# Kernel optimization log

Hardware: AMD Instinct MI355X
Metric: run time of the kernel (lower is better)

The kernel has to match this reference:

```python
import jax, jax.numpy as jnp
import numpy as np
import math

V, D, L, H, T, B = 32000, 1024, 4, 16, 2048, 1
HD = D // H
EPS = 1e-5

def _pos_encoding(T, D):
    pos = jnp.arange(T, dtype=jnp.float32)[:, None]                      # [T,1]
    div = jnp.exp(jnp.arange(0, D, 2, dtype=jnp.float32) * (-math.log(10000.0) / D))
    ang = pos * div                                                      # [T,D/2]
    pe = jnp.zeros((T, D), dtype=jnp.float32)
    pe = pe.at[:, 0::2].set(jnp.sin(ang)).at[:, 1::2].set(jnp.cos(ang))
    return pe

def _layernorm(x, g, b):
    mu = jnp.mean(x, axis=-1, keepdims=True)
    var = jnp.mean(jnp.square(x - mu), axis=-1, keepdims=True)
    return (x - mu) * jax.lax.rsqrt(var + EPS) * g + b

def setup_inputs() -> dict:
    key = jax.random.key(0)
    ks = jax.random.split(key, 16)
    s = 0.02
    inp = {
        'idx': jax.random.randint(ks[0], (B, T), 0, V),
        'embed': jax.random.normal(ks[1], (V, D), jnp.float32) * s,
        'Wq': jax.random.normal(ks[2], (L, D, D), jnp.float32) * s,
        'Wk': jax.random.normal(ks[3], (L, D, D), jnp.float32) * s,
        'Wv': jax.random.normal(ks[4], (L, D, D), jnp.float32) * s,
        'Wo': jax.random.normal(ks[5], (L, D, D), jnp.float32) * s,
        'bq': jnp.zeros((L, D), jnp.float32),
        'bk': jnp.zeros((L, D), jnp.float32),
        'bv': jnp.zeros((L, D), jnp.float32),
        'bo': jnp.zeros((L, D), jnp.float32),
        'ln1_g': jnp.ones((L, D), jnp.float32), 'ln1_b': jnp.zeros((L, D), jnp.float32),
        'ln2_g': jnp.ones((L, D), jnp.float32), 'ln2_b': jnp.zeros((L, D), jnp.float32),
        'w1': jax.random.normal(ks[6], (L, D, 4 * D), jnp.float32) * s,
        'b1': jnp.zeros((L, 4 * D), jnp.float32),
        'w2': jax.random.normal(ks[7], (L, 4 * D, D), jnp.float32) * s,
        'b2': jnp.zeros((L, D), jnp.float32),
        'lnf_g': jnp.ones((D,), jnp.float32), 'lnf_b': jnp.zeros((D,), jnp.float32),
        'head_w': jax.random.normal(ks[8], (D, V), jnp.float32) * s,
    }
    return inp

def _forward(idx, embed, Wq, Wk, Wv, Wo, bq, bk, bv, bo,
             ln1_g, ln1_b, ln2_g, ln2_b, w1, b1, w2, b2, lnf_g, lnf_b, head_w):
    Bs, Ts = idx.shape
    x = embed[idx] + _pos_encoding(Ts, embed.shape[1])[None]            # [B,T,D]
    causal = jnp.tril(jnp.ones((Ts, Ts), dtype=bool))                   # [T,T]
    scale = 1.0 / math.sqrt(HD)

    def block(x, p):
        wq, wk, wv, wo, q_b, k_b, v_b, o_b, g1, be1, g2, be2, fw1, fb1, fw2, fb2 = p
        h = _layernorm(x, g1, be1)
        q = (h @ wq + q_b).reshape(Bs, Ts, H, HD)
        k = (h @ wk + k_b).reshape(Bs, Ts, H, HD)
        v = (h @ wv + v_b).reshape(Bs, Ts, H, HD)
        att = jnp.einsum('bthd,bshd->bhts', q, k) * scale               # [B,H,T,T]
        att = jnp.where(causal, att, -jnp.inf)
        att = jax.nn.softmax(att, axis=-1)
        o = jnp.einsum('bhts,bshd->bthd', att, v).reshape(Bs, Ts, -1)
        x = x + (o @ wo + o_b)
        h2 = _layernorm(x, g2, be2)
        ff = jax.nn.gelu(h2 @ fw1 + fb1, approximate=False) @ fw2 + fb2
        x = x + ff
        return x, None

    params = (Wq, Wk, Wv, Wo, bq, bk, bv, bo, ln1_g, ln1_b, ln2_g, ln2_b, w1, b1, w2, b2)
    x, _ = jax.lax.scan(block, x, params)
    x = _layernorm(x, lnf_g, lnf_b)
    return x @ head_w                                                   # [B,T,V]

def reference(idx, embed, Wq, Wk, Wv, Wo, bq, bk, bv, bo,
              ln1_g, ln1_b, ln2_g, ln2_b, w1, b1, w2, b2, lnf_g, lnf_b, head_w):
    return _forward(idx, embed, Wq, Wk, Wv, Wo, bq, bk, bv, bo,
                    ln1_g, ln1_b, ln2_g, ln2_b, w1, b1, w2, b2, lnf_g, lnf_b, head_w)
```

## Files before the change

kernel.cpp:

```cpp
#include <hip/hip_runtime.h>
#include <cstdint>

using u16 = unsigned short;
using u32 = unsigned int;
typedef __bf16  bf16x8 __attribute__((ext_vector_type(8)));
typedef float   f32x4  __attribute__((ext_vector_type(4)));
typedef float   f32x16 __attribute__((ext_vector_type(16)));

__device__ __forceinline__ u16 f2b(float x) {
    u32 u = __builtin_bit_cast(u32, x);
    u = (u + 0x7fffu + ((u >> 16) & 1u)) >> 16;
    return (u16)u;
}

__device__ __forceinline__ f32x4 mfma16(bf16x8 a, bf16x8 b, f32x4 c) {
    return __builtin_amdgcn_mfma_f32_16x16x32_bf16(a, b, c, 0, 0, 0);
}
__device__ __forceinline__ f32x16 mfma32(bf16x8 a, bf16x8 b, f32x16 c) {
    return __builtin_amdgcn_mfma_f32_32x32x16_bf16(a, b, c, 0, 0, 0);
}

__device__ __forceinline__ void gload16(const void* g, void* lds) {
    auto gp = (__attribute__((address_space(1))) void*)(uintptr_t)g;
    auto lp = (__attribute__((address_space(3))) void*)(uintptr_t)lds;
    __builtin_amdgcn_global_load_lds(gp, lp, 16, 0, 0);
}

__device__ __forceinline__ int2 swz_bmbn(int nbm) {
    const int nwg = gridDim.x, orig = blockIdx.x;
    const int q = nwg >> 3, r = nwg & 7;
    const int xcd = orig & 7, lin = orig >> 3;
    const int id = (xcd < r ? xcd * (q + 1) : r * (q + 1) + (xcd - r) * q) + lin;
    return make_int2(id % nbm, id / nbm);
}

__global__ __launch_bounds__(512, 2) void gemm_head_k(
    const u16* __restrict__ A, const u16* __restrict__ Bt,
    float* __restrict__ out, int M, int N)
{
    constexpr int KV = 1024;
    constexpr int H  = KV >> 5;
    __shared__ __align__(16) u16 lsA[4][256 * 32];
    __shared__ __align__(16) u16 lsB[4][256 * 32];
    const int nbm = M >> 8;
    const int2 bb = swz_bmbn(nbm);
    const int m0 = bb.x * 256, n0 = bb.y * 256;
    const int tid = threadIdx.x;
    const int w = tid >> 6, lane = tid & 63;
    const int wr = (w >> 2) * 128, wc = (w & 3) * 64;
    const int lr = lane & 15, lg = lane >> 4;
    const int rsw = (lg ^ ((lr >> 1) & 3)) * 8;

    const int trow = tid >> 2;
    const int ksw8 = ((tid & 3) ^ ((tid >> 3) & 3)) * 8;
    const u16* aA = A  + (size_t)(m0 + trow) * KV + ksw8;
    const u16* aB = Bt + (size_t)(n0 + trow) * KV + ksw8;
    u16* dA = &lsA[0][0] + trow * 32 + (tid & 3) * 8;
    u16* dB = &lsB[0][0] + trow * 32 + (tid & 3) * 8;

    f32x4 acc[8][4] = {};

    auto stage = [&](int h) {
        const int sl = h & 3;
        const int ko = h * 32;
        gload16(aA + ko,                      dA + sl * 8192);
        gload16(aA + ko + (size_t)128 * KV,   dA + sl * 8192 + 4096);
        gload16(aB + ko,                      dB + sl * 8192);
        gload16(aB + ko + (size_t)128 * KV,   dB + sl * 8192 + 4096);
    };

    bf16x8 ra0[8], rb0[4], ra1[8], rb1[4];
    auto rdLow = [&](bf16x8* ra, bf16x8* rb, int h) {
        const int sl = h & 3;
#pragma unroll
        for (int m = 0; m < 4; m++)
            ra[m] = *(const bf16x8*)&lsA[sl][(wr + m * 16 + lr) * 32 + rsw];
#pragma unroll
        for (int n = 0; n < 4; n++)
            rb[n] = *(const bf16x8*)&lsB[sl][(wc + n * 16 + lr) * 32 + rsw];
    };
    auto rdHigh = [&](bf16x8* ra, int h) {
        const int sl = h & 3;
#pragma unroll
        for (int m = 4; m < 8; m++)
            ra[m] = *(const bf16x8*)&lsA[sl][(wr + m * 16 + lr) * 32 + rsw];
    };

    auto body = [&](int h, bf16x8* raC, bf16x8* rbC, bf16x8* raN, bf16x8* rbN) {
        rdHigh(raC, h);
        if (h + 3 < H) stage(h + 3);
        const int rem = H - 1 - h;
        if (rem >= 3)      asm volatile("s_waitcnt vmcnt(8)" ::: "memory");
        else if (rem == 2) asm volatile("s_waitcnt vmcnt(4)" ::: "memory");
        else if (rem == 1) asm volatile("s_waitcnt vmcnt(0)" ::: "memory");
        __builtin_amdgcn_s_barrier();
        asm volatile("s_waitcnt lgkmcnt(4)" ::: "memory");
        __builtin_amdgcn_sched_barrier(0);
        __builtin_amdgcn_s_setprio(1);
#pragma unroll
        for (int m = 0; m < 4; m++)
#pragma unroll
            for (int n = 0; n < 4; n++)
                acc[m][n] = mfma16(raC[m], rbC[n], acc[m][n]);
        __builtin_amdgcn_s_setprio(0);
        __builtin_amdgcn_sched_barrier(0);
        __builtin_amdgcn_s_barrier();
        if (h + 1 < H) rdLow(raN, rbN, h + 1);
        __builtin_amdgcn_sched_barrier(0);
        __builtin_amdgcn_s_barrier();
        if (h + 1 < H) asm volatile("s_waitcnt lgkmcnt(8)" ::: "memory");
        else           asm volatile("s_waitcnt lgkmcnt(0)" ::: "memory");
        __builtin_amdgcn_sched_barrier(0);
        __builtin_amdgcn_s_setprio(1);
#pragma unroll
        for (int m = 4; m < 8; m++)
#pragma unroll
            for (int n = 0; n < 4; n++)
                acc[m][n] = mfma16(raC[m], rbC[n], acc[m][n]);
        __builtin_amdgcn_s_setprio(0);
        __builtin_amdgcn_sched_barrier(0);
        __builtin_amdgcn_s_barrier();
    };

    stage(0); stage(1); stage(2);
    asm volatile("s_waitcnt vmcnt(8)" ::: "memory");
    __builtin_amdgcn_s_barrier();
    rdLow(ra0, rb0, 0);

#pragma unroll
    for (int h = 0; h < H; h += 2) {
        body(h,     ra0, rb0, ra1, rb1);
        body(h + 1, ra1, rb1, ra0, rb0);
    }

#pragma unroll
    for (int m = 0; m < 8; m++) {
        const int gr = m0 + wr + m * 16 + lg * 4;
#pragma unroll
        for (int r = 0; r < 4; r++) {
            float* orow = out + (size_t)(gr + r) * N + n0 + wc + lr;
#pragma unroll
            for (int n = 0; n < 4; n++)
                orow[n * 16] = acc[m][n][r];
        }
    }
}

template <int KC, int EPI>
__global__ __launch_bounds__(256, 2) void gemm_deep_k(
    const u16* __restrict__ A, int lda, const u16* __restrict__ Bt, int ldb,
    const float* __restrict__ bias, float* __restrict__ outf,
    u16* __restrict__ outb, int N, int nbm, int sk, long long sOut)
{
    constexpr int MF   = 4;
    constexpr int NF   = 4;
    constexpr int SLOT = 128 * 32;
    constexpr int HALF = 64 * 32;
    constexpr int H    = KC >> 5;

    __shared__ __align__(16) u16 lsA[4][SLOT];
    __shared__ __align__(16) u16 lsB[4][SLOT];

    const int s = blockIdx.y;
    A  += (size_t)s * sk;
    Bt += (size_t)s * sk;
    if (EPI == 4) outf += (size_t)s * sOut;

    const int2 bb = swz_bmbn(nbm);
    const int m0 = bb.x * 128, n0 = bb.y * 128;
    const int tid = threadIdx.x;
    const int w = tid >> 6, lane = tid & 63;
    const int wr = (w >> 1) * 64, wc = (w & 1) * 64;
    const int lr = lane & 15, lg = lane >> 4;
    const int rsw = (lg ^ ((lr >> 1) & 3)) * 8;

    const int trow = tid >> 2;
    const int ksw8 = ((tid & 3) ^ ((tid >> 3) & 3)) * 8;
    const u16* aA = A  + (size_t)(m0 + trow) * lda + ksw8;
    const u16* aB = Bt + (size_t)(n0 + trow) * ldb + ksw8;
    u16* dA = &lsA[0][0] + trow * 32 + (tid & 3) * 8;
    u16* dB = &lsB[0][0] + trow * 32 + (tid & 3) * 8;

    f32x4 acc[MF][NF] = {};

    auto stage = [&](int h) {
        const int sl = h & 3;
        const int koff = h * 32;
        gload16(aA + koff,                     dA + sl * SLOT);
        gload16(aA + koff + (size_t)64 * lda,  dA + sl * SLOT + HALF);
        gload16(aB + koff,                     dB + sl * SLOT);
        gload16(aB + koff + (size_t)64 * ldb,  dB + sl * SLOT + HALF);
    };

    bf16x8 ra0[MF], rb0[NF], ra1[MF], rb1[NF];
    auto lreadAll = [&](bf16x8* af, bf16x8* bf, int h) {
        const int sl = h & 3;
#pragma unroll
        for (int m = 0; m < MF; m++)
            af[m] = *(const bf16x8*)&lsA[sl][(wr + m * 16 + lr) * 32 + rsw];
#pragma unroll
        for (int n = 0; n < NF; n++)
            bf[n] = *(const bf16x8*)&lsB[sl][(wc + n * 16 + lr) * 32 + rsw];
    };

    auto body = [&](int h, bf16x8* aC, bf16x8* bC, bf16x8* aN, bf16x8* bN) {
        if (h + 3 < H) stage(h + 3);
        __builtin_amdgcn_sched_barrier(0);
        asm volatile("s_waitcnt lgkmcnt(0)" ::: "memory");
        const int rem = H - 1 - h;
        if (rem >= 3)      asm volatile("s_waitcnt vmcnt(8)" ::: "memory");
        else if (rem == 2) asm volatile("s_waitcnt vmcnt(4)" ::: "memory");
        else if (rem == 1) asm volatile("s_waitcnt vmcnt(0)" ::: "memory");
        __builtin_amdgcn_s_barrier();
        __builtin_amdgcn_sched_barrier(0);
        const int sl1 = (h + 1) & 3;
        const bool doRead = (h + 1 < H);
#pragma unroll
        for (int g = 0; g < 4; ++g) {
            if (doRead) {
#pragma unroll
                for (int t = g * 2; t < g * 2 + 2; ++t) {
                    if (t < MF) aN[t]      = *(const bf16x8*)&lsA[sl1][(wr + t * 16 + lr) * 32 + rsw];
                    else        bN[t - MF] = *(const bf16x8*)&lsB[sl1][(wc + (t - MF) * 16 + lr) * 32 + rsw];
                }
            }
            __builtin_amdgcn_sched_barrier(0);
            __builtin_amdgcn_s_setprio(1);
#pragma unroll
            for (int i = g * 4; i < g * 4 + 4; ++i)
                acc[i / NF][i % NF] = mfma16(aC[i / NF], bC[i % NF], acc[i / NF][i % NF]);
            __builtin_amdgcn_s_setprio(0);
            __builtin_amdgcn_sched_barrier(0);
        }
    };

    stage(0); stage(1); stage(2);
    asm volatile("s_waitcnt vmcnt(8)" ::: "memory");
    __builtin_amdgcn_s_barrier();
    lreadAll(ra0, rb0, 0);

#pragma unroll
    for (int h = 0; h < H; h += 2) {
        body(h,     ra0, rb0, ra1, rb1);
        body(h + 1, ra1, rb1, ra0, rb0);
    }

#pragma unroll
    for (int n = 0; n < NF; n++) {
        const int gc = n0 + wc + n * 16 + lr;
        float bv = 0.f;
        if constexpr (EPI == 0 || EPI == 1) bv = bias[gc];
#pragma unroll
        for (int m = 0; m < MF; m++) {
            const int grb = m0 + wr + m * 16 + lg * 4;
#pragma unroll
            for (int r = 0; r < 4; r++) {
                float v = acc[m][n][r] + bv;
                if constexpr (EPI == 1) v = 0.5f * v * (1.f + erff(v * 0.70710678118654752f));
                const size_t o = (size_t)(grb + r) * N + gc;
                if constexpr (EPI == 4) outf[o] = v;
                else                    outb[o] = f2b(v);
            }
        }
    }
}

__global__ __launch_bounds__(256) void reduce_ln_k(
    const float* __restrict__ pbuf, int S,
    const float* __restrict__ bias,
    float* __restrict__ x,
    const float* __restrict__ g, const float* __restrict__ bln,
    u16* __restrict__ hb)
{
    __shared__ float red[8];
    const int row = blockIdx.x, tid = threadIdx.x;
    const int w = tid >> 6, lane = tid & 63;
    const size_t base = (size_t)row * 256 + tid;
    float4 v = ((const float4*)x)[base];
    for (int s = 0; s < S; ++s) {
        const float4 p = ((const float4*)pbuf)[(size_t)s * 524288 + base];
        v.x += p.x; v.y += p.y; v.z += p.z; v.w += p.w;
    }
    const float4 bb = ((const float4*)bias)[tid];
    v.x += bb.x; v.y += bb.y; v.z += bb.z; v.w += bb.w;
    ((float4*)x)[base] = v;

    float s1 = v.x + v.y + v.z + v.w;
#pragma unroll
    for (int d = 1; d < 64; d <<= 1) s1 += __shfl_xor(s1, d);
    if (lane == 0) red[w] = s1;
    __syncthreads();
    const float mu = (red[0] + red[1] + red[2] + red[3]) * (1.f / 1024.f);
    const float d0 = v.x - mu, d1 = v.y - mu, d2 = v.z - mu, d3 = v.w - mu;
    float s2 = d0 * d0 + d1 * d1 + d2 * d2 + d3 * d3;
#pragma unroll
    for (int d = 1; d < 64; d <<= 1) s2 += __shfl_xor(s2, d);
    if (lane == 0) red[4 + w] = s2;
    __syncthreads();
    const float var = (red[4] + red[5] + red[6] + red[7]) * (1.f / 1024.f);
    const float rs = rsqrtf(var + 1e-5f);
    const float4 gv = ((const float4*)g)[tid];
    const float4 bv = ((const float4*)bln)[tid];
    u32 p0 = (u32)f2b(d0 * rs * gv.x + bv.x) | ((u32)f2b(d1 * rs * gv.y + bv.y) << 16);
    u32 p1 = (u32)f2b(d2 * rs * gv.z + bv.z) | ((u32)f2b(d3 * rs * gv.w + bv.w) << 16);
    ((uint2*)(hb + (size_t)row * 1024))[tid] = make_uint2(p0, p1);
}

__global__ __launch_bounds__(256) void flash_attn_k(
    const u16* __restrict__ qkv, const u16* __restrict__ vT, u16* __restrict__ out)
{
    constexpr int DS = 3072, T = 2048;
    __shared__ float mrg[2][64][32];
    __shared__ float msh[2][32], lsh[2][32];
    __shared__ u16   sbuf[2][32 * 68];
    const int w = threadIdx.x >> 6, lane = threadIdx.x & 63;
    const int lq = lane & 31, hi = lane >> 5;
    const int hoff = blockIdx.y * 64;
    const int pair = w >> 1, par = w & 1;
    const int qt = (pair == 0) ? blockIdx.x : 63 - blockIdx.x;
    const int q0 = qt * 32;
    const int qg = q0 + lq;

    const u16* qp = qkv + (size_t)qg * DS + hoff;
    const u16* kp = qkv + 1024 + hoff;

    bf16x8 qf[4];
#pragma unroll
    for (int d = 0; d < 4; d++)
        qf[d] = *(const bf16x8*)(qp + d * 16 + hi * 8);

    f32x16 o0 = {}, o1 = {};
    float m_r = -1e30f, l_r = 0.f;

    const int ntiles = (qt >> 1) + 1;
    for (int t = par; t < ntiles; t += 2) {
        const int kv0 = t * 64;
        f32x16 s0 = {}, s1 = {};
        {
            const u16* kb0 = kp + (size_t)(kv0 + lq) * DS + hi * 8;
            const u16* kb1 = kb0 + (size_t)32 * DS;
#pragma unroll
            for (int d = 0; d < 4; d++) {
                s0 = mfma32(*(const bf16x8*)(kb0 + d * 16), qf[d], s0);
                s1 = mfma32(*(const bf16x8*)(kb1 + d * 16), qf[d], s1);
            }
        }
        float p[32];
        float mx = -1e30f;
#pragma unroll
        for (int r = 0; r < 16; r++) {
            const int kvl = (r & 3) + 8 * (r >> 2) + 4 * hi;
            float v0 = (kv0 + kvl      <= qg) ? s0[r] * 0.125f : -1e30f;
            float v1 = (kv0 + 32 + kvl <= qg) ? s1[r] * 0.125f : -1e30f;
            p[r] = v0; p[16 + r] = v1;
            mx = fmaxf(mx, fmaxf(v0, v1));
        }
        mx = fmaxf(mx, __shfl_xor(mx, 32));
        const float mn = fmaxf(m_r, mx);
        const float alpha = __expf(m_r - mn);
        m_r = mn;
        float ls = 0.f;
#pragma unroll
        for (int i = 0; i < 32; i++) { p[i] = __expf(p[i] - mn); ls += p[i]; }
        ls += __shfl_xor(ls, 32);
        l_r = l_r * alpha + ls;
#pragma unroll
        for (int r = 0; r < 16; r++) { o0[r] *= alpha; o1[r] *= alpha; }
#pragma unroll
        for (int sub = 0; sub < 2; sub++) {
            u32 pw[8], x[8];
#pragma unroll
            for (int i = 0; i < 8; i++)
                pw[i] = (u32)f2b(p[sub * 16 + 2 * i]) | ((u32)f2b(p[sub * 16 + 2 * i + 1]) << 16);
#pragma unroll
            for (int i = 0; i < 8; i++) x[i] = __shfl_xor(pw[i], 32);
            u32 b0[4], b1[4];
            b0[0] = hi ? x[2]  : pw[0];  b0[1] = hi ? x[3]  : pw[1];
            b0[2] = hi ? pw[2] : x[0];   b0[3] = hi ? pw[3] : x[1];
            b1[0] = hi ? x[6]  : pw[4];  b1[1] = hi ? x[7]  : pw[5];
            b1[2] = hi ? pw[6] : x[4];   b1[3] = hi ? pw[7] : x[5];
            bf16x8 B0 = __builtin_bit_cast(bf16x8, *(const uint4*)b0);
            bf16x8 B1 = __builtin_bit_cast(bf16x8, *(const uint4*)b1);
            const u16* vb = vT + (size_t)(hoff + lq) * T + kv0 + sub * 32 + hi * 8;
            o0 = mfma32(*(const bf16x8*)vb, B0, o0);
            o0 = mfma32(*(const bf16x8*)(vb + 16), B1, o0);
            const u16* vb1 = vb + (size_t)32 * T;
            o1 = mfma32(*(const bf16x8*)vb1, B0, o1);
            o1 = mfma32(*(const bf16x8*)(vb1 + 16), B1, o1);
        }
    }

    __syncthreads();
    if (par == 0) {
#pragma unroll
        for (int r = 0; r < 16; r++) {
            const int d = (r & 3) + 8 * (r >> 2) + 4 * hi;
            mrg[pair][d][lq]      = o0[r];
            mrg[pair][d + 32][lq] = o1[r];
        }
        if (hi == 0) { msh[pair][lq] = m_r; lsh[pair][lq] = l_r; }
    }
    __syncthreads();
    if (par == 1) {
        const float m0v = msh[pair][lq], l0v = lsh[pair][lq];
        const float M = fmaxf(m0v, m_r);
        const float f0 = __expf(m0v - M), f1 = __expf(m_r - M);
        const float linv = 1.f / (l0v * f0 + l_r * f1);
        u32* sb = (u32*)sbuf[pair];
#pragma unroll
        for (int r = 0; r < 16; r += 2) {
            const int d = (r & 3) + 8 * (r >> 2) + 4 * hi;
            float va = (mrg[pair][d][lq] * f0 + o0[r] * f1) * linv;
            float vb = (mrg[pair][d + 1][lq] * f0 + o0[r + 1] * f1) * linv;
            sb[lq * 34 + (d >> 1)] = (u32)f2b(va) | ((u32)f2b(vb) << 16);
            float vc = (mrg[pair][d + 32][lq] * f0 + o1[r] * f1) * linv;
            float vd = (mrg[pair][d + 33][lq] * f0 + o1[r + 1] * f1) * linv;
            sb[lq * 34 + ((d + 32) >> 1)] = (u32)f2b(vc) | ((u32)f2b(vd) << 16);
        }
#pragma unroll
        for (int ps = 0; ps < 8; ps++) {
            const int row = ps * 4 + (lane >> 4);
            const uint2 v = *(const uint2*)&sbuf[pair][row * 68 + (lane & 15) * 4];
            *(uint2*)(out + (size_t)(q0 + row) * 1024 + hoff + (lane & 15) * 4) = v;
        }
    }
}

__global__ __launch_bounds__(256) void transpose_cvt_k(
    const float* __restrict__ src, u16* __restrict__ dst, int K, int N,
    long long srcLS, long long dstLS)
{
    __shared__ float tf[32][132];
    src += (size_t)blockIdx.z * srcLS;
    dst += (size_t)blockIdx.z * dstLS;
    const int n0 = blockIdx.x * 128, k0 = blockIdx.y * 32;
    const int tid = threadIdx.x;
    const int tn = tid & 31, tk = tid >> 5;
#pragma unroll
    for (int p = 0; p < 4; ++p) {
        const int k = tk + p * 8;
        const float4 v = *(const float4*)&src[(size_t)(k0 + k) * N + n0 + tn * 4];
        *(float4*)&tf[k][tn * 4] = v;
    }
    __syncthreads();
    const int kq = (tid & 7) * 4;
    const int tn2 = tid >> 3;
#pragma unroll
    for (int w = 0; w < 4; ++w) {
        const int n = tn2 + w * 32;
        const u32 lo = (u32)f2b(tf[kq + 0][n]) | ((u32)f2b(tf[kq + 1][n]) << 16);
        const u32 hi = (u32)f2b(tf[kq + 2][n]) | ((u32)f2b(tf[kq + 3][n]) << 16);
        *(uint2*)&dst[(size_t)(n0 + n) * K + k0 + kq] = make_uint2(lo, hi);
    }
}

__global__ __launch_bounds__(256) void transpose_u16_k(
    const u16* __restrict__ src, u16* __restrict__ dst, int R, int C, int srcStride)
{
    __shared__ u16 tile[32][33];
    const int c0 = blockIdx.x * 32, r0 = blockIdx.y * 32;
    const int tx = threadIdx.x & 31, ty = threadIdx.x >> 5;
#pragma unroll
    for (int r = 0; r < 32; r += 8)
        tile[ty + r][tx] = src[(size_t)(r0 + ty + r) * srcStride + c0 + tx];
    __syncthreads();
#pragma unroll
    for (int r = 0; r < 32; r += 8)
        dst[(size_t)(c0 + ty + r) * R + r0 + tx] = tile[tx][ty + r];
}

__global__ __launch_bounds__(256) void concat_bias_k(
    const float* __restrict__ bq, const float* __restrict__ bk,
    const float* __restrict__ bv, float* __restrict__ bcat)
{
    const int l = blockIdx.y;
    const int j = blockIdx.x * 256 + threadIdx.x;
    float v;
    if (j < 1024)      v = bq[l * 1024 + j];
    else if (j < 2048) v = bk[l * 1024 + j - 1024];
    else               v = bv[l * 1024 + j - 2048];
    bcat[l * 3072 + j] = v;
}

__global__ __launch_bounds__(256) void embed_pos_k(
    const int* __restrict__ idx, const float* __restrict__ emb, float* __restrict__ x)
{
    const int t = blockIdx.x, tid = threadIdx.x;
    const int tok = idx[t];
    float4 e = ((const float4*)(emb + (size_t)tok * 1024))[tid];
    const int d0 = tid * 4;
    const float c = -0.0089944730195080f;
    const float a0 = (float)t * expf((float)d0 * c);
    const float a1 = (float)t * expf((float)(d0 + 2) * c);
    e.x += sinf(a0); e.y += cosf(a0); e.z += sinf(a1); e.w += cosf(a1);
    ((float4*)(x + (size_t)t * 1024))[tid] = e;
}

__global__ __launch_bounds__(256) void layernorm_k(
    const float* __restrict__ x, const float* __restrict__ g,
    const float* __restrict__ b, u16* __restrict__ out)
{
    __shared__ float red[8];
    const int row = blockIdx.x, tid = threadIdx.x;
    const int w = tid >> 6, lane = tid & 63;
    const float4 v = ((const float4*)(x + (size_t)row * 1024))[tid];
    float s = v.x + v.y + v.z + v.w;
#pragma unroll
    for (int d = 1; d < 64; d <<= 1) s += __shfl_xor(s, d);
    if (lane == 0) red[w] = s;
    __syncthreads();
    const float mu = (red[0] + red[1] + red[2] + red[3]) * (1.f / 1024.f);
    const float d0 = v.x - mu, d1 = v.y - mu, d2 = v.z - mu, d3 = v.w - mu;
    float s2 = d0 * d0 + d1 * d1 + d2 * d2 + d3 * d3;
#pragma unroll
    for (int d = 1; d < 64; d <<= 1) s2 += __shfl_xor(s2, d);
    if (lane == 0) red[4 + w] = s2;
    __syncthreads();
    const float var = (red[4] + red[5] + red[6] + red[7]) * (1.f / 1024.f);
    const float rs = rsqrtf(var + 1e-5f);
    const float4 gv = ((const float4*)g)[tid];
    const float4 bv = ((const float4*)b)[tid];
    u32 p0 = (u32)f2b(d0 * rs * gv.x + bv.x) | ((u32)f2b(d1 * rs * gv.y + bv.y) << 16);
    u32 p1 = (u32)f2b(d2 * rs * gv.z + bv.z) | ((u32)f2b(d3 * rs * gv.w + bv.w) << 16);
    ((uint2*)(out + (size_t)row * 1024))[tid] = make_uint2(p0, p1);
}

extern "C" void kernel_launch(void* const* d_in, const int* in_sizes, int n_in,
                              void* d_out, int out_size, void* d_ws, size_t ws_size,
                              hipStream_t stream)
{
    const int*   idx   = (const int*)  d_in[0];
    const float* embed = (const float*)d_in[1];
    const float* Wq    = (const float*)d_in[2];
    const float* Wk    = (const float*)d_in[3];
    const float* Wv    = (const float*)d_in[4];
    const float* Wo    = (const float*)d_in[5];
    const float* bq    = (const float*)d_in[6];
    const float* bk    = (const float*)d_in[7];
    const float* bv    = (const float*)d_in[8];
    const float* bo    = (const float*)d_in[9];
    const float* ln1g  = (const float*)d_in[10];
    const float* ln1b  = (const float*)d_in[11];
    const float* ln2g  = (const float*)d_in[12];
    const float* ln2b  = (const float*)d_in[13];
    const float* w1    = (const float*)d_in[14];
    const float* b1    = (const float*)d_in[15];
    const float* w2    = (const float*)d_in[16];
    const float* b2    = (const float*)d_in[17];
    const float* lnfg  = (const float*)d_in[18];
    const float* lnfb  = (const float*)d_in[19];
    const float* headw = (const float*)d_in[20];

    char* ws = (char*)d_ws;
    auto alloc = [&](size_t bytes) {
        char* p = ws;
        ws += (bytes + 255) & ~(size_t)255;
        return p;
    };
    u16*   qkvT = (u16*)alloc((size_t)4 * 3072 * 1024 * 2);
    u16*   WoT  = (u16*)alloc((size_t)4 * 1024 * 1024 * 2);
    u16*   w1T  = (u16*)alloc((size_t)4 * 1024 * 4096 * 2);
    u16*   w2T  = (u16*)alloc((size_t)4 * 1024 * 4096 * 2);
    u16*   hT   = (u16*)alloc((size_t)32000 * 1024 * 2);
    float* bcat = (float*)alloc((size_t)4 * 3072 * 4);
    float* x    = (float*)alloc((size_t)2048 * 1024 * 4);
    u16*   hb   = (u16*)alloc((size_t)2048 * 1024 * 2);
    u16*   qkvb = (u16*)alloc((size_t)2048 * 3072 * 2);
    u16*   vTb  = (u16*)alloc((size_t)2048 * 1024 * 2);
    u16*   ab   = (u16*)alloc((size_t)2048 * 1024 * 2);
    u16*   ff   = (u16*)alloc((size_t)2048 * 4096 * 2);
    float* pbuf = (float*)d_out;

    transpose_cvt_k<<<dim3(8, 32, 4),   256, 0, stream>>>(Wq, qkvT,            1024, 1024, 1048576, 3145728);
    transpose_cvt_k<<<dim3(8, 32, 4),   256, 0, stream>>>(Wk, qkvT + 1048576,  1024, 1024, 1048576, 3145728);
    transpose_cvt_k<<<dim3(8, 32, 4),   256, 0, stream>>>(Wv, qkvT + 2097152,  1024, 1024, 1048576, 3145728);
    transpose_cvt_k<<<dim3(8, 32, 4),   256, 0, stream>>>(Wo, WoT,             1024, 1024, 1048576, 1048576);
    transpose_cvt_k<<<dim3(32, 32, 4),  256, 0, stream>>>(w1, w1T,             1024, 4096, 4194304, 4194304);
    transpose_cvt_k<<<dim3(8, 128, 4),  256, 0, stream>>>(w2, w2T,             4096, 1024, 4194304, 4194304);
    transpose_cvt_k<<<dim3(250, 32, 1), 256, 0, stream>>>(headw, hT,           1024, 32000, 0, 0);
    concat_bias_k<<<dim3(12, 4), 256, 0, stream>>>(bq, bk, bv, bcat);

    embed_pos_k<<<dim3(2048), 256, 0, stream>>>(idx, embed, x);
    layernorm_k<<<dim3(2048), 256, 0, stream>>>(x, ln1g, ln1b, hb);

    for (int l = 0; l < 4; ++l) {
        gemm_deep_k<1024, 0><<<dim3(384), 256, 0, stream>>>(
            hb, 1024, qkvT + (size_t)l * 3145728, 1024,
            bcat + l * 3072, nullptr, qkvb, 3072, 16, 0, 0);
        transpose_u16_k<<<dim3(32, 64), 256, 0, stream>>>(qkvb + 2048, vTb, 2048, 1024, 3072);
        flash_attn_k<<<dim3(32, 16), 256, 0, stream>>>(qkvb, vTb, ab);
        gemm_deep_k<512, 4><<<dim3(128, 2), 256, 0, stream>>>(
            ab, 1024, WoT + (size_t)l * 1048576, 1024,
            nullptr, pbuf, nullptr, 1024, 16, 512, 2097152);
        reduce_ln_k<<<dim3(2048), 256, 0, stream>>>(pbuf, 2, bo + l * 1024, x,
                                                    ln2g + l * 1024, ln2b + l * 1024, hb);
        gemm_deep_k<1024, 1><<<dim3(512), 256, 0, stream>>>(
            hb, 1024, w1T + (size_t)l * 4194304, 1024,
            b1 + l * 4096, nullptr, ff, 4096, 16, 0, 0);
        gemm_deep_k<1024, 4><<<dim3(128, 4), 256, 0, stream>>>(
            ff, 4096, w2T + (size_t)l * 4194304, 4096,
            nullptr, pbuf, nullptr, 1024, 16, 1024, 2097152);
        const float* ng = (l < 3) ? (ln1g + (l + 1) * 1024) : lnfg;
        const float* nb = (l < 3) ? (ln1b + (l + 1) * 1024) : lnfb;
        reduce_ln_k<<<dim3(2048), 256, 0, stream>>>(pbuf, 4, b2 + l * 1024, x, ng, nb, hb);
    }
    gemm_head_k<<<dim3(1000), 512, 0, stream>>>(hb, hT, (float*)d_out, 2048, 32000);
}
```

Measured before the change: 975.8 us.

## Simplify GEMM main-loop scheduling and fuse embedding with first layernorm

Both GEMM kernels drop their hand-interleaved LDS-read/MFMA schedule, with its split halves, extra barriers and sched_barrier groups. Each iteration now reads the whole next fragment set and then issues all MFMAs in one block, leaving the interleaving to the compiler. Separately, the embedding+positional-encoding kernel is fused with the first layernorm, which saves one launch and a reread of x. The simpler GEMM schedule removes barrier overhead but may lose the explicit overlap of LDS reads with matrix ops.

```diff
diff --git a/kernel.cpp b/kernel.cpp
--- a/kernel.cpp
+++ b/kernel.cpp
@@ -70,62 +70,42 @@
     };
 
     bf16x8 ra0[8], rb0[4], ra1[8], rb1[4];
-    auto rdLow = [&](bf16x8* ra, bf16x8* rb, int h) {
+    auto lread = [&](bf16x8* af, bf16x8* bf, int h) {
         const int sl = h & 3;
 #pragma unroll
-        for (int m = 0; m < 4; m++)
-            ra[m] = *(const bf16x8*)&lsA[sl][(wr + m * 16 + lr) * 32 + rsw];
+        for (int m = 0; m < 8; m++)
+            af[m] = *(const bf16x8*)&lsA[sl][(wr + m * 16 + lr) * 32 + rsw];
 #pragma unroll
         for (int n = 0; n < 4; n++)
-            rb[n] = *(const bf16x8*)&lsB[sl][(wc + n * 16 + lr) * 32 + rsw];
-    };
-    auto rdHigh = [&](bf16x8* ra, int h) {
-        const int sl = h & 3;
-#pragma unroll
-        for (int m = 4; m < 8; m++)
-            ra[m] = *(const bf16x8*)&lsA[sl][(wr + m * 16 + lr) * 32 + rsw];
-    };
-
-    auto body = [&](int h, bf16x8* raC, bf16x8* rbC, bf16x8* raN, bf16x8* rbN) {
-        rdHigh(raC, h);
+            bf[n] = *(const bf16x8*)&lsB[sl][(wc + n * 16 + lr) * 32 + rsw];
+    };
+    auto mm = [&](bf16x8* af, bf16x8* bf) {
+        __builtin_amdgcn_s_setprio(1);
+#pragma unroll
+        for (int m = 0; m < 8; m++)
+#pragma unroll
+            for (int n = 0; n < 4; n++)
+                acc[m][n] = mfma16(af[m], bf[n], acc[m][n]);
+        __builtin_amdgcn_s_setprio(0);
+    };
+
+    auto body = [&](int h, bf16x8* aC, bf16x8* bC, bf16x8* aN, bf16x8* bN) {
         if (h + 3 < H) stage(h + 3);
+        asm volatile("s_waitcnt lgkmcnt(0)" ::: "memory");
         const int rem = H - 1 - h;
         if (rem >= 3)      asm volatile("s_waitcnt vmcnt(8)" ::: "memory");
         else if (rem == 2) asm volatile("s_waitcnt vmcnt(4)" ::: "memory");
         else if (rem == 1) asm volatile("s_waitcnt vmcnt(0)" ::: "memory");
         __builtin_amdgcn_s_barrier();
-        asm volatile("s_waitcnt lgkmcnt(4)" ::: "memory");
         __builtin_amdgcn_sched_barrier(0);
-        __builtin_amdgcn_s_setprio(1);
-#pragma unroll
-        for (int m = 0; m < 4; m++)
-#pragma unroll
-            for (int n = 0; n < 4; n++)
-                acc[m][n] = mfma16(raC[m], rbC[n], acc[m][n]);
-        __builtin_amdgcn_s_setprio(0);
-        __builtin_amdgcn_sched_barrier(0);
-        __builtin_amdgcn_s_barrier();
-        if (h + 1 < H) rdLow(raN, rbN, h + 1);
-        __builtin_amdgcn_sched_barrier(0);
-        __builtin_amdgcn_s_barrier();
-        if (h + 1 < H) asm volatile("s_waitcnt lgkmcnt(8)" ::: "memory");
-        else           asm volatile("s_waitcnt lgkmcnt(0)" ::: "memory");
-        __builtin_amdgcn_sched_barrier(0);
-        __builtin_amdgcn_s_setprio(1);
-#pragma unroll
-        for (int m = 4; m < 8; m++)
-#pragma unroll
-            for (int n = 0; n < 4; n++)
-                acc[m][n] = mfma16(raC[m], rbC[n], acc[m][n]);
-        __builtin_amdgcn_s_setprio(0);
-        __builtin_amdgcn_sched_barrier(0);
-        __builtin_amdgcn_s_barrier();
+        if (h + 1 < H) lread(aN, bN, h + 1);
+        mm(aC, bC);
     };
 
     stage(0); stage(1); stage(2);
     asm volatile("s_waitcnt vmcnt(8)" ::: "memory");
     __builtin_amdgcn_s_barrier();
-    rdLow(ra0, rb0, 0);
+    lread(ra0, rb0, 0);
 
 #pragma unroll
     for (int h = 0; h < H; h += 2) {
@@ -193,7 +173,7 @@
     };
 
     bf16x8 ra0[MF], rb0[NF], ra1[MF], rb1[NF];
-    auto lreadAll = [&](bf16x8* af, bf16x8* bf, int h) {
+    auto lread = [&](bf16x8* af, bf16x8* bf, int h) {
         const int sl = h & 3;
 #pragma unroll
         for (int m = 0; m < MF; m++)
@@ -205,7 +185,6 @@
 
     auto body = [&](int h, bf16x8* aC, bf16x8* bC, bf16x8* aN, bf16x8* bN) {
         if (h + 3 < H) stage(h + 3);
-        __builtin_amdgcn_sched_barrier(0);
         asm volatile("s_waitcnt lgkmcnt(0)" ::: "memory");
         const int rem = H - 1 - h;
         if (rem >= 3)      asm volatile("s_waitcnt vmcnt(8)" ::: "memory");
@@ -213,31 +192,20 @@
         else if (rem == 1) asm volatile("s_waitcnt vmcnt(0)" ::: "memory");
         __builtin_amdgcn_s_barrier();
         __builtin_amdgcn_sched_barrier(0);
-        const int sl1 = (h + 1) & 3;
-        const bool doRead = (h + 1 < H);
-#pragma unroll
-        for (int g = 0; g < 4; ++g) {
-            if (doRead) {
-#pragma unroll
-                for (int t = g * 2; t < g * 2 + 2; ++t) {
-                    if (t < MF) aN[t]      = *(const bf16x8*)&lsA[sl1][(wr + t * 16 + lr) * 32 + rsw];
-                    else        bN[t - MF] = *(const bf16x8*)&lsB[sl1][(wc + (t - MF) * 16 + lr) * 32 + rsw];
-                }
-            }
-            __builtin_amdgcn_sched_barrier(0);
-            __builtin_amdgcn_s_setprio(1);
-#pragma unroll
-            for (int i = g * 4; i < g * 4 + 4; ++i)
-                acc[i / NF][i % NF] = mfma16(aC[i / NF], bC[i % NF], acc[i / NF][i % NF]);
-            __builtin_amdgcn_s_setprio(0);
-            __builtin_amdgcn_sched_barrier(0);
-        }
+        if (h + 1 < H) lread(aN, bN, h + 1);
+        __builtin_amdgcn_s_setprio(1);
+#pragma unroll
+        for (int m = 0; m < MF; m++)
+#pragma unroll
+            for (int n = 0; n < NF; n++)
+                acc[m][n] = mfma16(aC[m], bC[n], acc[m][n]);
+        __builtin_amdgcn_s_setprio(0);
     };
 
     stage(0); stage(1); stage(2);
     asm volatile("s_waitcnt vmcnt(8)" ::: "memory");
     __builtin_amdgcn_s_barrier();
-    lreadAll(ra0, rb0, 0);
+    lread(ra0, rb0, 0);
 
 #pragma unroll
     for (int h = 0; h < H; h += 2) {
@@ -482,32 +450,27 @@
     bcat[l * 3072 + j] = v;
 }
 
-__global__ __launch_bounds__(256) void embed_pos_k(
-    const int* __restrict__ idx, const float* __restrict__ emb, float* __restrict__ x)
-{
+__global__ __launch_bounds__(256) void embed_ln_k(
+    const int* __restrict__ idx, const float* __restrict__ emb,
+    const float* __restrict__ g, const float* __restrict__ b,
+    float* __restrict__ x, u16* __restrict__ out)
+{
+    __shared__ float red[8];
     const int t = blockIdx.x, tid = threadIdx.x;
+    const int w = tid >> 6, lane = tid & 63;
     const int tok = idx[t];
-    float4 e = ((const float4*)(emb + (size_t)tok * 1024))[tid];
-    const int d0 = tid * 4;
+    float4 v = ((const float4*)(emb + (size_t)tok * 1024))[tid];
+    const int d0i = tid * 4;
     const float c = -0.0089944730195080f;
-    const float a0 = (float)t * expf((float)d0 * c);
-    const float a1 = (float)t * expf((float)(d0 + 2) * c);
-    e.x += sinf(a0); e.y += cosf(a0); e.z += sinf(a1); e.w += cosf(a1);
-    ((float4*)(x + (size_t)t * 1024))[tid] = e;
-}
-
-__global__ __launch_bounds__(256) void layernorm_k(
-    const float* __restrict__ x, const float* __restrict__ g,
-    const float* __restrict__ b, u16* __restrict__ out)
-{
-    __shared__ float red[8];
-    const int row = blockIdx.x, tid = threadIdx.x;
-    const int w = tid >> 6, lane = tid & 63;
-    const float4 v = ((const float4*)(x + (size_t)row * 1024))[tid];
-    float s = v.x + v.y + v.z + v.w;
-#pragma unroll
-    for (int d = 1; d < 64; d <<= 1) s += __shfl_xor(s, d);
-    if (lane == 0) red[w] = s;
+    const float a0 = (float)t * expf((float)d0i * c);
+    const float a1 = (float)t * expf((float)(d0i + 2) * c);
+    v.x += sinf(a0); v.y += cosf(a0); v.z += sinf(a1); v.w += cosf(a1);
+    ((float4*)(x + (size_t)t * 1024))[tid] = v;
+
+    float s1 = v.x + v.y + v.z + v.w;
+#pragma unroll
+    for (int d = 1; d < 64; d <<= 1) s1 += __shfl_xor(s1, d);
+    if (lane == 0) red[w] = s1;
     __syncthreads();
     const float mu = (red[0] + red[1] + red[2] + red[3]) * (1.f / 1024.f);
     const float d0 = v.x - mu, d1 = v.y - mu, d2 = v.z - mu, d3 = v.w - mu;
@@ -522,7 +485,7 @@
     const float4 bv = ((const float4*)b)[tid];
     u32 p0 = (u32)f2b(d0 * rs * gv.x + bv.x) | ((u32)f2b(d1 * rs * gv.y + bv.y) << 16);
     u32 p1 = (u32)f2b(d2 * rs * gv.z + bv.z) | ((u32)f2b(d3 * rs * gv.w + bv.w) << 16);
-    ((uint2*)(out + (size_t)row * 1024))[tid] = make_uint2(p0, p1);
+    ((uint2*)(out + (size_t)t * 1024))[tid] = make_uint2(p0, p1);
 }
 
 extern "C" void kernel_launch(void* const* d_in, const int* in_sizes, int n_in,
@@ -580,8 +543,7 @@
     transpose_cvt_k<<<dim3(250, 32, 1), 256, 0, stream>>>(headw, hT,           1024, 32000, 0, 0);
     concat_bias_k<<<dim3(12, 4), 256, 0, stream>>>(bq, bk, bv, bcat);
 
-    embed_pos_k<<<dim3(2048), 256, 0, stream>>>(idx, embed, x);
-    layernorm_k<<<dim3(2048), 256, 0, stream>>>(x, ln1g, ln1b, hb);
+    embed_ln_k<<<dim3(2048), 256, 0, stream>>>(idx, embed, ln1g, ln1b, x, hb);
 
     for (int l = 0; l < 4; ++l) {
         gemm_deep_k<1024, 0><<<dim3(384), 256, 0, stream>>>(
```

New measurement: 961.3 us. About the same (-1.5%).
